# Kernel optimization log

Measured on AMD Instinct MI355X. Metric: run time of the kernel, lower is better.

The kernel has to match this reference:

```python
import jax, jax.numpy as jnp
import numpy as np

B, T, DIM, H, DH, DT = 2, 2048, 1024, 16, 64, 32
Q_TEMP, K_TEMP = 1.0, 1.0
EPS = float(np.finfo(np.float32).eps)  # torch RMSNorm default eps for fp32
INV_SQRT_DH = 1.0 / np.sqrt(DH)


def _get_time(length, head_time_delta, time_angles, with_time_delta):
    # [T,1,1] positions, optionally offset per head -> [T,H,1]
    pos = jnp.arange(length, dtype=jnp.float32)[:, None, None]
    if with_time_delta:
        pos = pos + head_time_delta[None, :, None]          # [T,H,1]
    else:
        pos = jnp.broadcast_to(pos, (length, H, 1))          # [T,H,1]
    ang = pos * time_angles                                  # [T,H,Dt]
    c, s = jnp.cos(ang), jnp.sin(ang)
    return jnp.concatenate([c + s, c - s], axis=-1) * INV_SQRT_DH  # [T,H,2Dt]


def setup_inputs() -> dict:
    key = jax.random.key(0)
    ks = jax.random.split(key, 6)
    sc = 0.02
    states = jax.random.normal(ks[0], (B, T, DIM), jnp.float32)
    attention_mask = jnp.ones((B, T), jnp.int32)
    ln_w = jnp.ones((DIM,), jnp.float32)
    time_angles = 10000.0 ** (-1.0 / jnp.arange(1, DT + 1, dtype=jnp.float32))
    head_time_delta = jax.random.uniform(ks[1], (H,), jnp.float32)
    Wq = jax.random.normal(ks[2], (H * DH, DIM), jnp.float32) * sc
    q_bias = jnp.zeros((H * DH,), jnp.float32)
    Wk = jax.random.normal(ks[3], (H * DH, DIM), jnp.float32) * sc
    bk = jnp.zeros((H * DH,), jnp.float32)
    Wv = jax.random.normal(ks[4], (H * DH, DIM), jnp.float32) * sc
    bv = jnp.zeros((H * DH,), jnp.float32)
    Wo = jax.random.normal(ks[5], (DIM, H * DH), jnp.float32) * sc
    bo = jnp.zeros((DIM,), jnp.float32)
    return dict(states=states, attention_mask=attention_mask, ln_w=ln_w,
                time_angles=time_angles, head_time_delta=head_time_delta,
                Wq=Wq, q_bias=q_bias, Wk=Wk, bk=bk, Wv=Wv, bv=bv, Wo=Wo, bo=bo)


def reference(states, attention_mask, ln_w, time_angles, head_time_delta,
              Wq, q_bias, Wk, bk, Wv, bv, Wo, bo):
    # RMSNorm
    x = states * jax.lax.rsqrt(jnp.mean(states * states, axis=-1, keepdims=True) + EPS) * ln_w
    m = attention_mask.astype(x.dtype)[:, :, None, None]   # [B,T,1,1]

    # Q path -> q_attentioned [B,T,T,H]
    q = (x @ Wq.T - jnp.exp(q_bias)).reshape(B, T, H, DH)
    q_sm = jax.nn.softmax(q / Q_TEMP * m, axis=-1)
    t_q = _get_time(T, head_time_delta, time_angles, True)   # [T,H,2Dt]
    t_k = _get_time(T, head_time_delta, time_angles, False)  # [T,H,2Dt]
    q_timed = jnp.sum(q_sm, axis=-1, keepdims=True) * t_q    # [B,T,H,2Dt]
    q_att = jnp.einsum('bthd,lhd->btlh', q_timed, t_k)       # [B,T,T,H]

    # KV path
    k = (x @ Wk.T + bk).reshape(B, T, H, DH)
    k_sm = jax.nn.softmax(k / K_TEMP * m, axis=-1)
    v = (x @ Wv.T + bv).reshape(B, T, H, DH)
    kv = k_sm * v                                            # [B,T,H,Dh]

    loading = jnp.einsum('btlh,blhd->bthd', q_att, kv)       # [B,T,H,Dh]
    return loading.reshape(B, T, DIM) @ Wo.T + bo
```

## Files before the change

kernel.cpp:

```cpp
#include <hip/hip_runtime.h>
#include <math.h>

#define T_ 2048
#define H_ 16

typedef __attribute__((ext_vector_type(8))) short bfx8;
typedef __attribute__((ext_vector_type(4))) float f32x4;

__device__ __forceinline__ short f2bf(float f) {
  union { float f; unsigned u; } x; x.f = f;
  unsigned r = (x.u + 0x7FFFu + ((x.u >> 16) & 1u)) >> 16;
  return (short)r;
}
__device__ __forceinline__ float bf2f(short s) {
  union { unsigned u; float f; } x;
  x.u = ((unsigned)(unsigned short)s) << 16;
  return x.f;
}

#define GLD_LDS(g, l) \
  __builtin_amdgcn_global_load_lds( \
      (const __attribute__((address_space(1))) void*)(g), \
      (__attribute__((address_space(3))) void*)(l), 16, 0, 0)

__global__ __launch_bounds__(256) void prep_kernel(
    const float* __restrict__ Wk, const float* __restrict__ Wv,
    const float* __restrict__ Wo, const float* __restrict__ angles,
    const float* __restrict__ states, const float* __restrict__ ln_w,
    short* __restrict__ Wkb, short* __restrict__ Wvb, short* __restrict__ Wob,
    short* __restrict__ xb, short* __restrict__ Cb, short* __restrict__ tkT,
    float* __restrict__ MtH) {
  const int blk = blockIdx.x;
  if (blk < 3072) {
    const int i = blk * 256 + threadIdx.x;
    const int which = i >> 18;
    const int idx = i & 262143;
    const float* s = (which == 0) ? Wk : (which == 1) ? Wv : Wo;
    short* d = (which == 0) ? Wkb : (which == 1) ? Wvb : Wob;
    const float4 v = ((const float4*)s)[idx];
    short4 r;
    r.x = f2bf(v.x); r.y = f2bf(v.y); r.z = f2bf(v.z); r.w = f2bf(v.w);
    ((short4*)d)[idx] = r;
  } else if (blk < 7168) {
    const int row = blk - 3072;
    const int tid = threadIdx.x;
    const float4 v = ((const float4*)(states + (size_t)row * 1024))[tid];
    float ss = v.x * v.x + v.y * v.y + v.z * v.z + v.w * v.w;
#pragma unroll
    for (int off = 32; off >= 1; off >>= 1) ss += __shfl_xor(ss, off);
    __shared__ float red[4];
    if ((tid & 63) == 0) red[tid >> 6] = ss;
    __syncthreads();
    const float tot = red[0] + red[1] + red[2] + red[3];
    const float scale = rsqrtf(tot * (1.0f / 1024.0f) + 1.1920928955078125e-07f);
    const float4 w = ((const float4*)ln_w)[tid];
    short4 o;
    o.x = f2bf(v.x * scale * w.x);
    o.y = f2bf(v.y * scale * w.y);
    o.z = f2bf(v.z * scale * w.z);
    o.w = f2bf(v.w * scale * w.w);
    ((short4*)(xb + (size_t)row * 1024))[tid] = o;
  } else if (blk < 7424) {
    const int gid = (blk - 7168) * 256 + threadIdx.x;
    const int j = gid & 31;
    const int t = gid >> 5;
    float s, c;
    sincosf((float)t * angles[j], &s, &c);
    Cb[(size_t)t * 64 + j] = f2bf(0.125f * c);
    Cb[(size_t)t * 64 + 32 + j] = f2bf(0.125f * s);
  } else if (blk < 7456) {
    const int gid = (blk - 7424) * 256 + threadIdx.x;
    const int tc = gid & 255;
    const int j = gid >> 8;
    const float th = angles[j];
    short lo[8], hi[8];
#pragma unroll
    for (int r = 0; r < 8; ++r) {
      float s, c;
      sincosf((float)(tc * 8 + r) * th, &s, &c);
      lo[r] = f2bf((c + s) * 0.125f);
      hi[r] = f2bf((c - s) * 0.125f);
    }
    short* base = tkT + (size_t)j * 2048 + tc * 8;
    *(short4*)(base) = *(short4*)&lo[0];
    *(short4*)(base + 4) = *(short4*)&lo[4];
    short* base2 = tkT + (size_t)(32 + j) * 2048 + tc * 8;
    *(short4*)(base2) = *(short4*)&hi[0];
    *(short4*)(base2 + 4) = *(short4*)&hi[4];
  } else {
    const int gid = (blk - 7456) * 256 + threadIdx.x;
    ((float4*)MtH)[gid] = make_float4(0.f, 0.f, 0.f, 0.f);
  }
}

__global__ __launch_bounds__(256) void kvgemm_kernel(
    const short* __restrict__ xb, const short* __restrict__ Wkb,
    const short* __restrict__ Wvb, const float* __restrict__ bk,
    const float* __restrict__ bv, const int* __restrict__ mask,
    const short* __restrict__ tkT, float* __restrict__ Mt) {
  __shared__ short smem[16384];
  __shared__ short Vs[128][64];
  short(*As)[64] = (short(*)[64])smem;
  short(*Bk)[64] = (short(*)[64])(smem + 8192);
  short(*Bv)[64] = (short(*)[64])(smem + 12288);
  short(*kvS)[132] = (short(*)[132])smem;

  const int row0 = blockIdx.x * 128;
  const int h = blockIdx.y;
  const int t = threadIdx.x;
  const int lane = t & 63;
  const int wv = t >> 6;
  const bool isV = wv >= 2;
  const int wrow = (wv & 1) * 64;
  const int lrow = lane & 15;

  const int srow8 = t >> 3;
  const int kslotS = (t & 7) ^ (srow8 & 7);
  const short* gaS = xb + (size_t)(row0 + srow8) * 1024 + kslotS * 8;
  const short* gkS = Wkb + (size_t)(h * 64 + srow8) * 1024 + kslotS * 8;
  const short* gvS = Wvb + (size_t)(h * 64 + srow8) * 1024 + kslotS * 8;
  short* laS = &As[srow8][(t & 7) * 8];
  short* lkS = &Bk[srow8][(t & 7) * 8];
  short* lvS = &Bv[srow8][(t & 7) * 8];

  f32x4 acc[4][4] = {};
  for (int k0 = 0; k0 < 1024; k0 += 64) {
    GLD_LDS(gaS + k0, laS);
    GLD_LDS(gaS + 32 * 1024 + k0, laS + 2048);
    GLD_LDS(gaS + 64 * 1024 + k0, laS + 4096);
    GLD_LDS(gaS + 96 * 1024 + k0, laS + 6144);
    GLD_LDS(gkS + k0, lkS);
    GLD_LDS(gkS + 32 * 1024 + k0, lkS + 2048);
    GLD_LDS(gvS + k0, lvS);
    GLD_LDS(gvS + 32 * 1024 + k0, lvS + 2048);
    __syncthreads();
#pragma unroll
    for (int kk = 0; kk < 2; ++kk) {
      const int pcol = ((kk * 4 + (lane >> 4)) ^ (lrow & 7)) * 8;
      bfx8 af[4], bf_[4];
#pragma unroll
      for (int i = 0; i < 4; ++i)
        af[i] = *(const bfx8*)&As[wrow + i * 16 + lrow][pcol];
      const short(*Bs)[64] = isV ? Bv : Bk;
#pragma unroll
      for (int j = 0; j < 4; ++j)
        bf_[j] = *(const bfx8*)&Bs[j * 16 + lrow][pcol];
#pragma unroll
      for (int i = 0; i < 4; ++i)
#pragma unroll
        for (int j = 0; j < 4; ++j)
          acc[i][j] = __builtin_amdgcn_mfma_f32_16x16x32_bf16(af[i], bf_[j], acc[i][j], 0, 0, 0);
    }
    __syncthreads();
  }
  const int rq = (lane >> 4) * 4;
  if (isV) {
#pragma unroll
    for (int j = 0; j < 4; ++j) {
      const float bb = bv[h * 64 + j * 16 + lrow];
#pragma unroll
      for (int i = 0; i < 4; ++i)
#pragma unroll
        for (int rr = 0; rr < 4; ++rr)
          Vs[wrow + rq + i * 16 + rr][j * 16 + lrow] = f2bf(acc[i][j][rr] + bb);
    }
  }
  __syncthreads();
  if (!isV) {
    float bkc[4];
#pragma unroll
    for (int j = 0; j < 4; ++j) bkc[j] = bk[h * 64 + j * 16 + lrow];
    const int rowg0 = row0 + wrow + rq;
#pragma unroll
    for (int i = 0; i < 4; ++i) {
#pragma unroll
      for (int rr = 0; rr < 4; ++rr) {
        const float m = (float)mask[rowg0 + i * 16 + rr];
        float kf[4];
#pragma unroll
        for (int j = 0; j < 4; ++j) kf[j] = (acc[i][j][rr] + bkc[j]) * m;
        float mx = fmaxf(fmaxf(kf[0], kf[1]), fmaxf(kf[2], kf[3]));
#pragma unroll
        for (int off = 8; off >= 1; off >>= 1) mx = fmaxf(mx, __shfl_xor(mx, off));
        float s = 0.0f;
#pragma unroll
        for (int j = 0; j < 4; ++j) { kf[j] = expf(kf[j] - mx); s += kf[j]; }
#pragma unroll
        for (int off = 8; off >= 1; off >>= 1) s += __shfl_xor(s, off);
        const float inv = 1.0f / s;
#pragma unroll
        for (int j = 0; j < 4; ++j)
          acc[i][j][rr] = kf[j] * inv *
                          bf2f(Vs[wrow + rq + i * 16 + rr][j * 16 + lrow]);
      }
    }
#pragma unroll
    for (int j = 0; j < 4; ++j) {
      const int d = j * 16 + lrow;
#pragma unroll
      for (int i = 0; i < 4; ++i) {
        short4 o;
        o.x = f2bf(acc[i][j][0]); o.y = f2bf(acc[i][j][1]);
        o.z = f2bf(acc[i][j][2]); o.w = f2bf(acc[i][j][3]);
        *(short4*)&kvS[d][wrow + rq + i * 16] = o;
      }
    }
  }
  __syncthreads();
  const int bb = row0 >> 11;
  const int tb = row0 & 2047;
  const short* tkb = tkT + (size_t)(wv * 16 + lrow) * 2048 + tb;
  const int kg = (lane >> 4) * 8;
  f32x4 macc[4] = {};
#pragma unroll
  for (int kc = 0; kc < 4; ++kc) {
    const bfx8 af = *(const bfx8*)(tkb + kc * 32 + kg);
#pragma unroll
    for (int j = 0; j < 4; ++j) {
      const bfx8 bf_ = *(const bfx8*)&kvS[j * 16 + lrow][kc * 32 + kg];
      macc[j] = __builtin_amdgcn_mfma_f32_16x16x32_bf16(af, bf_, macc[j], 0, 0, 0);
    }
  }
  float* Mb = Mt + (size_t)(bb * 16 + h) * 4096;
#pragma unroll
  for (int j = 0; j < 4; ++j) {
    const int d = j * 16 + lrow;
#pragma unroll
    for (int rr = 0; rr < 4; ++rr) {
      const int e = wv * 16 + rq + rr;
      atomicAdd(&Mb[(size_t)e * 64 + d], macc[j][rr]);
    }
  }
}

__global__ __launch_bounds__(256) void fold_kernel(
    const float* __restrict__ Mt, const float* __restrict__ angles,
    const float* __restrict__ delta, short* __restrict__ Mf) {
  const int bh = blockIdx.x;
  const int b = bh >> 4, h = bh & 15;
  const int t = threadIdx.x;
  const int j = t >> 3;
  const int d8 = (t & 7) * 8;
  float sphi, cphi;
  sincosf(delta[h] * angles[j], &sphi, &cphi);
  const float p = cphi + sphi, q = cphi - sphi;
  const float* m0 = Mt + (size_t)bh * 4096 + (size_t)j * 64 + d8;
  const float* m1 = Mt + (size_t)bh * 4096 + (size_t)(32 + j) * 64 + d8;
  short* oc = Mf + (size_t)b * 65536 + (size_t)j * 1024 + h * 64 + d8;
  short* os = Mf + (size_t)b * 65536 + (size_t)(32 + j) * 1024 + h * 64 + d8;
#pragma unroll
  for (int c = 0; c < 8; ++c) {
    const float a = m0[c], bb = m1[c];
    oc[c] = f2bf(p * a + q * bb);
    os[c] = f2bf(q * a - p * bb);
  }
}

__global__ __launch_bounds__(256) void hgemm_kernel(
    const short* __restrict__ Wob, const short* __restrict__ Mf,
    float* __restrict__ H) {
  const int kc = blockIdx.x;
  const int o0 = blockIdx.y * 64;
  const int b = blockIdx.z;
  const int t = threadIdx.x;
  const int lane = t & 63;
  const int w = t >> 6;
  const int lrow = lane & 15;
  const int kg = (lane >> 4) * 8;
  const int orow = o0 + w * 16 + lrow;
  f32x4 acc[4] = {};
#pragma unroll
  for (int it = 0; it < 4; ++it) {
    const int kb = kc * 128 + it * 32 + kg;
    const bfx8 af = *(const bfx8*)(Wob + (size_t)orow * 1024 + kb);
#pragma unroll
    for (int j = 0; j < 4; ++j) {
      const bfx8 bf_ = *(const bfx8*)(Mf + (size_t)b * 65536 +
                                      (size_t)(j * 16 + lrow) * 1024 + kb);
      acc[j] = __builtin_amdgcn_mfma_f32_16x16x32_bf16(af, bf_, acc[j], 0, 0, 0);
    }
  }
  float* Hb = H + (size_t)b * 65536;
#pragma unroll
  for (int j = 0; j < 4; ++j) {
    const int kap = j * 16 + lrow;
#pragma unroll
    for (int rr = 0; rr < 4; ++rr) {
      const int o = o0 + w * 16 + (lane >> 4) * 4 + rr;
      atomicAdd(&Hb[(size_t)o * 64 + kap], acc[j][rr]);
    }
  }
}

__global__ __launch_bounds__(256) void ofinal_kernel(
    const short* __restrict__ Cb, const float* __restrict__ H,
    const float* __restrict__ bo, float* __restrict__ out) {
  const int col0 = blockIdx.x * 128;
  const int row0 = blockIdx.y * 128;
  const int b = blockIdx.z;
  float* C = out + (size_t)b * 2097152;
  const float* Hb = H + (size_t)b * 65536;
  const int t = threadIdx.x;
  const int lane = t & 63;
  const int wv = t >> 6;
  const int wm = (wv & 1) * 64, wn = (wv >> 1) * 64;
  const int lrow = lane & 15;
  const int kg = (lane >> 4) * 8;
  f32x4 acc[4][4] = {};
#pragma unroll
  for (int k0 = 0; k0 < 64; k0 += 32) {
    bfx8 af[4], bf_[4];
#pragma unroll
    for (int i = 0; i < 4; ++i)
      af[i] = *(const bfx8*)(Cb + (size_t)(row0 + wm + i * 16 + lrow) * 64 + k0 + kg);
#pragma unroll
    for (int j = 0; j < 4; ++j) {
      const float* hp = Hb + (size_t)(col0 + wn + j * 16 + lrow) * 64 + k0 + kg;
      const float4 h0 = *(const float4*)hp;
      const float4 h1 = *(const float4*)(hp + 4);
      bfx8 bb;
      bb[0] = f2bf(h0.x); bb[1] = f2bf(h0.y); bb[2] = f2bf(h0.z); bb[3] = f2bf(h0.w);
      bb[4] = f2bf(h1.x); bb[5] = f2bf(h1.y); bb[6] = f2bf(h1.z); bb[7] = f2bf(h1.w);
      bf_[j] = bb;
    }
#pragma unroll
    for (int i = 0; i < 4; ++i)
#pragma unroll
      for (int j = 0; j < 4; ++j)
        acc[i][j] = __builtin_amdgcn_mfma_f32_16x16x32_bf16(af[i], bf_[j], acc[i][j], 0, 0, 0);
  }
  const int rq = (lane >> 4) * 4;
#pragma unroll
  for (int j = 0; j < 4; ++j) {
    const int c = col0 + wn + j * 16 + lrow;
    const float bb = bo[c];
#pragma unroll
    for (int i = 0; i < 4; ++i) {
      const int r = row0 + wm + i * 16 + rq;
#pragma unroll
      for (int rr = 0; rr < 4; ++rr)
        C[(size_t)(r + rr) * 1024 + c] = acc[i][j][rr] + bb;
    }
  }
}

extern "C" void kernel_launch(void* const* d_in, const int* in_sizes, int n_in,
                              void* d_out, int out_size, void* d_ws, size_t ws_size,
                              hipStream_t stream) {
  (void)in_sizes; (void)n_in; (void)out_size; (void)ws_size;
  const float* states = (const float*)d_in[0];
  const int* mask = (const int*)d_in[1];
  const float* ln_w = (const float*)d_in[2];
  const float* angles = (const float*)d_in[3];
  const float* delta = (const float*)d_in[4];
  const float* Wk = (const float*)d_in[7];
  const float* bk = (const float*)d_in[8];
  const float* Wv = (const float*)d_in[9];
  const float* bv = (const float*)d_in[10];
  const float* Wo = (const float*)d_in[11];
  const float* bo = (const float*)d_in[12];
  float* out = (float*)d_out;

  char* W = (char*)d_ws;
  short* xb  = (short*)(W);
  short* Wkb = (short*)(W + (8u << 20));
  short* Wvb = (short*)(W + (10u << 20));
  short* Wob = (short*)(W + (12u << 20));
  short* Cb  = (short*)(W + (14u << 20));
  short* tkT = (short*)(W + (14u << 20) + (256u << 10));
  short* Mf  = (short*)(W + (14u << 20) + (512u << 10));
  float* Mt  = (float*)(W + (15u << 20));
  float* H   = (float*)(W + (15u << 20) + (512u << 10));

  prep_kernel<<<7712, 256, 0, stream>>>(Wk, Wv, Wo, angles, states, ln_w,
                                        Wkb, Wvb, Wob, xb, Cb, tkT, Mt);
  kvgemm_kernel<<<dim3(32, 16), 256, 0, stream>>>(xb, Wkb, Wvb, bk, bv, mask,
                                                  tkT, Mt);
  fold_kernel<<<32, 256, 0, stream>>>(Mt, angles, delta, Mf);
  hgemm_kernel<<<dim3(8, 16, 2), 256, 0, stream>>>(Wob, Mf, H);
  ofinal_kernel<<<dim3(8, 16, 2), 256, 0, stream>>>(Cb, H, bo, out);
}
```

Before: 145.0 us.

## Halve kvgemm row tile to 64 and split head columns across waves

The K/V GEMM block now covers 64 rows instead of 128, doubling the grid to 64x16 blocks. Each wave computes half of the 64 head columns, so the per-row softmax is split across two waves and combined through shared-memory max and sum reductions with extra barriers. The aim is more blocks in flight (512 blocks was few for the device's CUs) and smaller LDS use per block. In exchange, each block reloads the Wk/Wv tiles for fewer rows, adds synchronisation steps, and doubles the atomicAdd traffic into Mt.

```diff
diff --git a/kernel.cpp b/kernel.cpp
--- a/kernel.cpp
+++ b/kernel.cpp
@@ -98,21 +98,24 @@
     const short* __restrict__ Wvb, const float* __restrict__ bk,
     const float* __restrict__ bv, const int* __restrict__ mask,
     const short* __restrict__ tkT, float* __restrict__ Mt) {
-  __shared__ short smem[16384];
-  __shared__ short Vs[128][64];
+  __shared__ short smem[12288];
+  __shared__ float redM[2][64];
+  __shared__ float redS[2][64];
   short(*As)[64] = (short(*)[64])smem;
-  short(*Bk)[64] = (short(*)[64])(smem + 8192);
-  short(*Bv)[64] = (short(*)[64])(smem + 12288);
-  short(*kvS)[132] = (short(*)[132])smem;
-
-  const int row0 = blockIdx.x * 128;
+  short(*Bk)[64] = (short(*)[64])(smem + 4096);
+  short(*Bv)[64] = (short(*)[64])(smem + 8192);
+  short(*Vs)[64] = (short(*)[64])smem;
+  short(*kvS)[68] = (short(*)[68])(smem + 4096);
+
+  const int row0 = blockIdx.x * 64;
   const int h = blockIdx.y;
   const int t = threadIdx.x;
   const int lane = t & 63;
   const int wv = t >> 6;
   const bool isV = wv >= 2;
-  const int wrow = (wv & 1) * 64;
+  const int whalf = wv & 1;
   const int lrow = lane & 15;
+  const int quad = lane >> 4;
 
   const int srow8 = t >> 3;
   const int kslotS = (t & 7) ^ (srow8 & 7);
@@ -123,12 +126,10 @@
   short* lkS = &Bk[srow8][(t & 7) * 8];
   short* lvS = &Bv[srow8][(t & 7) * 8];
 
-  f32x4 acc[4][4] = {};
+  f32x4 acc[4][2] = {};
   for (int k0 = 0; k0 < 1024; k0 += 64) {
     GLD_LDS(gaS + k0, laS);
     GLD_LDS(gaS + 32 * 1024 + k0, laS + 2048);
-    GLD_LDS(gaS + 64 * 1024 + k0, laS + 4096);
-    GLD_LDS(gaS + 96 * 1024 + k0, laS + 6144);
     GLD_LDS(gkS + k0, lkS);
     GLD_LDS(gkS + 32 * 1024 + k0, lkS + 2048);
     GLD_LDS(gvS + k0, lvS);
@@ -136,73 +137,90 @@
     __syncthreads();
 #pragma unroll
     for (int kk = 0; kk < 2; ++kk) {
-      const int pcol = ((kk * 4 + (lane >> 4)) ^ (lrow & 7)) * 8;
-      bfx8 af[4], bf_[4];
+      const int pcol = ((kk * 4 + quad) ^ (lrow & 7)) * 8;
+      bfx8 af[4], bf_[2];
 #pragma unroll
       for (int i = 0; i < 4; ++i)
-        af[i] = *(const bfx8*)&As[wrow + i * 16 + lrow][pcol];
+        af[i] = *(const bfx8*)&As[i * 16 + lrow][pcol];
       const short(*Bs)[64] = isV ? Bv : Bk;
 #pragma unroll
-      for (int j = 0; j < 4; ++j)
-        bf_[j] = *(const bfx8*)&Bs[j * 16 + lrow][pcol];
+      for (int j = 0; j < 2; ++j)
+        bf_[j] = *(const bfx8*)&Bs[whalf * 32 + j * 16 + lrow][pcol];
 #pragma unroll
       for (int i = 0; i < 4; ++i)
 #pragma unroll
-        for (int j = 0; j < 4; ++j)
+        for (int j = 0; j < 2; ++j)
           acc[i][j] = __builtin_amdgcn_mfma_f32_16x16x32_bf16(af[i], bf_[j], acc[i][j], 0, 0, 0);
     }
     __syncthreads();
   }
-  const int rq = (lane >> 4) * 4;
   if (isV) {
 #pragma unroll
-    for (int j = 0; j < 4; ++j) {
-      const float bb = bv[h * 64 + j * 16 + lrow];
+    for (int j = 0; j < 2; ++j) {
+      const float bb = bv[h * 64 + whalf * 32 + j * 16 + lrow];
 #pragma unroll
       for (int i = 0; i < 4; ++i)
 #pragma unroll
         for (int rr = 0; rr < 4; ++rr)
-          Vs[wrow + rq + i * 16 + rr][j * 16 + lrow] = f2bf(acc[i][j][rr] + bb);
+          Vs[quad * 4 + i * 16 + rr][whalf * 32 + j * 16 + lrow] =
+              f2bf(acc[i][j][rr] + bb);
+    }
+  } else {
+    float bkc[2];
+#pragma unroll
+    for (int j = 0; j < 2; ++j) bkc[j] = bk[h * 64 + whalf * 32 + j * 16 + lrow];
+#pragma unroll
+    for (int i = 0; i < 4; ++i) {
+#pragma unroll
+      for (int rr = 0; rr < 4; ++rr) {
+        const int row = quad * 4 + i * 16 + rr;
+        const float m = (float)mask[row0 + row];
+        const float k0v = (acc[i][0][rr] + bkc[0]) * m;
+        const float k1v = (acc[i][1][rr] + bkc[1]) * m;
+        acc[i][0][rr] = k0v;
+        acc[i][1][rr] = k1v;
+        float mx = fmaxf(k0v, k1v);
+#pragma unroll
+        for (int off = 8; off >= 1; off >>= 1) mx = fmaxf(mx, __shfl_xor(mx, off));
+        if (lrow == 0) redM[whalf][row] = mx;
+      }
     }
   }
   __syncthreads();
   if (!isV) {
-    float bkc[4];
-#pragma unroll
-    for (int j = 0; j < 4; ++j) bkc[j] = bk[h * 64 + j * 16 + lrow];
-    const int rowg0 = row0 + wrow + rq;
 #pragma unroll
     for (int i = 0; i < 4; ++i) {
 #pragma unroll
       for (int rr = 0; rr < 4; ++rr) {
-        const float m = (float)mask[rowg0 + i * 16 + rr];
-        float kf[4];
-#pragma unroll
-        for (int j = 0; j < 4; ++j) kf[j] = (acc[i][j][rr] + bkc[j]) * m;
-        float mx = fmaxf(fmaxf(kf[0], kf[1]), fmaxf(kf[2], kf[3]));
-#pragma unroll
-        for (int off = 8; off >= 1; off >>= 1) mx = fmaxf(mx, __shfl_xor(mx, off));
-        float s = 0.0f;
-#pragma unroll
-        for (int j = 0; j < 4; ++j) { kf[j] = expf(kf[j] - mx); s += kf[j]; }
+        const int row = quad * 4 + i * 16 + rr;
+        const float mx = fmaxf(redM[0][row], redM[1][row]);
+        const float e0 = expf(acc[i][0][rr] - mx);
+        const float e1 = expf(acc[i][1][rr] - mx);
+        acc[i][0][rr] = e0;
+        acc[i][1][rr] = e1;
+        float s = e0 + e1;
 #pragma unroll
         for (int off = 8; off >= 1; off >>= 1) s += __shfl_xor(s, off);
-        const float inv = 1.0f / s;
-#pragma unroll
-        for (int j = 0; j < 4; ++j)
-          acc[i][j][rr] = kf[j] * inv *
-                          bf2f(Vs[wrow + rq + i * 16 + rr][j * 16 + lrow]);
+        if (lrow == 0) redS[whalf][row] = s;
       }
     }
-#pragma unroll
-    for (int j = 0; j < 4; ++j) {
-      const int d = j * 16 + lrow;
+  }
+  __syncthreads();
+  if (!isV) {
+#pragma unroll
+    for (int j = 0; j < 2; ++j) {
+      const int d = whalf * 32 + j * 16 + lrow;
 #pragma unroll
       for (int i = 0; i < 4; ++i) {
         short4 o;
-        o.x = f2bf(acc[i][j][0]); o.y = f2bf(acc[i][j][1]);
-        o.z = f2bf(acc[i][j][2]); o.w = f2bf(acc[i][j][3]);
-        *(short4*)&kvS[d][wrow + rq + i * 16] = o;
+        short* op = (short*)&o;
+#pragma unroll
+        for (int rr = 0; rr < 4; ++rr) {
+          const int row = quad * 4 + i * 16 + rr;
+          const float inv = 1.0f / (redS[0][row] + redS[1][row]);
+          op[rr] = f2bf(acc[i][j][rr] * inv * bf2f(Vs[row][d]));
+        }
+        *(short4*)&kvS[d][quad * 4 + i * 16] = o;
       }
     }
   }
@@ -210,10 +228,10 @@
   const int bb = row0 >> 11;
   const int tb = row0 & 2047;
   const short* tkb = tkT + (size_t)(wv * 16 + lrow) * 2048 + tb;
-  const int kg = (lane >> 4) * 8;
+  const int kg = quad * 8;
   f32x4 macc[4] = {};
 #pragma unroll
-  for (int kc = 0; kc < 4; ++kc) {
+  for (int kc = 0; kc < 2; ++kc) {
     const bfx8 af = *(const bfx8*)(tkb + kc * 32 + kg);
 #pragma unroll
     for (int j = 0; j < 4; ++j) {
@@ -227,7 +245,7 @@
     const int d = j * 16 + lrow;
 #pragma unroll
     for (int rr = 0; rr < 4; ++rr) {
-      const int e = wv * 16 + rq + rr;
+      const int e = wv * 16 + quad * 4 + rr;
       atomicAdd(&Mb[(size_t)e * 64 + d], macc[j][rr]);
     }
   }
@@ -374,7 +392,7 @@
 
   prep_kernel<<<7712, 256, 0, stream>>>(Wk, Wv, Wo, angles, states, ln_w,
                                         Wkb, Wvb, Wob, xb, Cb, tkT, Mt);
-  kvgemm_kernel<<<dim3(32, 16), 256, 0, stream>>>(xb, Wkb, Wvb, bk, bv, mask,
+  kvgemm_kernel<<<dim3(64, 16), 256, 0, stream>>>(xb, Wkb, Wvb, bk, bv, mask,
                                                   tkT, Mt);
   fold_kernel<<<32, 256, 0, stream>>>(Mt, angles, delta, Mf);
   hgemm_kernel<<<dim3(8, 16, 2), 256, 0, stream>>>(Wob, Mf, H);
```

Result: slower. 170.7 us (+17.7%).

## Load GEMM operands directly from global into registers with double buffering

Applied to the files above, without the earlier changes.

The K/V projection GEMM no longer stages A and B tiles through LDS with global_load_lds and block barriers. Each wave now loads its MFMA fragments straight from global memory into registers and double-buffers them across 32 k-steps, which removes the __syncthreads and the LDS round trip. The cost is that data shared between waves is fetched redundantly from global or L2. The loads are also 16-byte gathers with a 2 KB row stride, so coalescing is worse and register pressure rises.

```diff
diff --git a/kernel.cpp b/kernel.cpp
--- a/kernel.cpp
+++ b/kernel.cpp
@@ -17,11 +17,6 @@
   x.u = ((unsigned)(unsigned short)s) << 16;
   return x.f;
 }
-
-#define GLD_LDS(g, l) \
-  __builtin_amdgcn_global_load_lds( \
-      (const __attribute__((address_space(1))) void*)(g), \
-      (__attribute__((address_space(3))) void*)(l), 16, 0, 0)
 
 __global__ __launch_bounds__(256) void prep_kernel(
     const float* __restrict__ Wk, const float* __restrict__ Wv,
@@ -98,12 +93,8 @@
     const short* __restrict__ Wvb, const float* __restrict__ bk,
     const float* __restrict__ bv, const int* __restrict__ mask,
     const short* __restrict__ tkT, float* __restrict__ Mt) {
-  __shared__ short smem[16384];
   __shared__ short Vs[128][64];
-  short(*As)[64] = (short(*)[64])smem;
-  short(*Bk)[64] = (short(*)[64])(smem + 8192);
-  short(*Bv)[64] = (short(*)[64])(smem + 12288);
-  short(*kvS)[132] = (short(*)[132])smem;
+  __shared__ short kvS[64][132];
 
   const int row0 = blockIdx.x * 128;
   const int h = blockIdx.y;
@@ -113,47 +104,36 @@
   const bool isV = wv >= 2;
   const int wrow = (wv & 1) * 64;
   const int lrow = lane & 15;
-
-  const int srow8 = t >> 3;
-  const int kslotS = (t & 7) ^ (srow8 & 7);
-  const short* gaS = xb + (size_t)(row0 + srow8) * 1024 + kslotS * 8;
-  const short* gkS = Wkb + (size_t)(h * 64 + srow8) * 1024 + kslotS * 8;
-  const short* gvS = Wvb + (size_t)(h * 64 + srow8) * 1024 + kslotS * 8;
-  short* laS = &As[srow8][(t & 7) * 8];
-  short* lkS = &Bk[srow8][(t & 7) * 8];
-  short* lvS = &Bv[srow8][(t & 7) * 8];
+  const int quad = lane >> 4;
+
+  const short* Ab = xb + (size_t)(row0 + wrow + lrow) * 1024 + quad * 8;
+  const short* Bb = (isV ? Wvb : Wkb) + (size_t)(h * 64 + lrow) * 1024 + quad * 8;
 
   f32x4 acc[4][4] = {};
-  for (int k0 = 0; k0 < 1024; k0 += 64) {
-    GLD_LDS(gaS + k0, laS);
-    GLD_LDS(gaS + 32 * 1024 + k0, laS + 2048);
-    GLD_LDS(gaS + 64 * 1024 + k0, laS + 4096);
-    GLD_LDS(gaS + 96 * 1024 + k0, laS + 6144);
-    GLD_LDS(gkS + k0, lkS);
-    GLD_LDS(gkS + 32 * 1024 + k0, lkS + 2048);
-    GLD_LDS(gvS + k0, lvS);
-    GLD_LDS(gvS + 32 * 1024 + k0, lvS + 2048);
-    __syncthreads();
-#pragma unroll
-    for (int kk = 0; kk < 2; ++kk) {
-      const int pcol = ((kk * 4 + (lane >> 4)) ^ (lrow & 7)) * 8;
-      bfx8 af[4], bf_[4];
-#pragma unroll
-      for (int i = 0; i < 4; ++i)
-        af[i] = *(const bfx8*)&As[wrow + i * 16 + lrow][pcol];
-      const short(*Bs)[64] = isV ? Bv : Bk;
+  bfx8 aF[2][4], bF[2][4];
+#pragma unroll
+  for (int i = 0; i < 4; ++i) {
+    aF[0][i] = *(const bfx8*)(Ab + (size_t)i * 16384);
+    bF[0][i] = *(const bfx8*)(Bb + (size_t)i * 16384);
+  }
+#pragma unroll
+  for (int it = 0; it < 32; ++it) {
+    const int cur = it & 1, nxt = cur ^ 1;
+    if (it < 31) {
+      const int k1 = (it + 1) * 32;
+#pragma unroll
+      for (int i = 0; i < 4; ++i) {
+        aF[nxt][i] = *(const bfx8*)(Ab + (size_t)i * 16384 + k1);
+        bF[nxt][i] = *(const bfx8*)(Bb + (size_t)i * 16384 + k1);
+      }
+    }
+#pragma unroll
+    for (int i = 0; i < 4; ++i)
 #pragma unroll
       for (int j = 0; j < 4; ++j)
-        bf_[j] = *(const bfx8*)&Bs[j * 16 + lrow][pcol];
-#pragma unroll
-      for (int i = 0; i < 4; ++i)
-#pragma unroll
-        for (int j = 0; j < 4; ++j)
-          acc[i][j] = __builtin_amdgcn_mfma_f32_16x16x32_bf16(af[i], bf_[j], acc[i][j], 0, 0, 0);
-    }
-    __syncthreads();
-  }
-  const int rq = (lane >> 4) * 4;
+        acc[i][j] = __builtin_amdgcn_mfma_f32_16x16x32_bf16(aF[cur][i], bF[cur][j], acc[i][j], 0, 0, 0);
+  }
+  const int rq = quad * 4;
   if (isV) {
 #pragma unroll
     for (int j = 0; j < 4; ++j) {
@@ -210,7 +190,7 @@
   const int bb = row0 >> 11;
   const int tb = row0 & 2047;
   const short* tkb = tkT + (size_t)(wv * 16 + lrow) * 2048 + tb;
-  const int kg = (lane >> 4) * 8;
+  const int kg = quad * 8;
   f32x4 macc[4] = {};
 #pragma unroll
   for (int kc = 0; kc < 4; ++kc) {
```

Result: slower. 185.1 us (+27.7%).
